# Optimization experiments

Measured on AMD Instinct MI355X. Metric: run time of the kernel, lower is better.

The kernel has to match this reference:

```python
import jax, jax.numpy as jnp
import numpy as np

D_MODEL = 1024
N_HEAD = 16
D_K = D_MODEL // N_HEAD
D_FF = 2048
N_EXPERTS = 8
TOP_K = 2
B = 4
S = 1024
LN_EPS = 1e-5


def _layer_norm(x, g, b):
    mu = jnp.mean(x, axis=-1, keepdims=True)
    var = jnp.mean(jnp.square(x - mu), axis=-1, keepdims=True)
    return (x - mu) * jax.lax.rsqrt(var + LN_EPS) * g + b


def setup_inputs() -> dict:
    key = jax.random.key(0)
    ks = jax.random.split(key, 16)
    std = 0.02
    inp = {
        "x": jax.random.normal(ks[0], (B, S, D_MODEL), dtype=jnp.float32),
        "mask": jnp.ones((B, S, S), dtype=jnp.int32),
        "ln1_g": jnp.ones((D_MODEL,), jnp.float32),
        "ln1_b": jnp.zeros((D_MODEL,), jnp.float32),
        "wq": jax.random.normal(ks[1], (D_MODEL, D_MODEL), jnp.float32) * std,
        "wk": jax.random.normal(ks[2], (D_MODEL, D_MODEL), jnp.float32) * std,
        "wv": jax.random.normal(ks[3], (D_MODEL, D_MODEL), jnp.float32) * std,
        "wo": jax.random.normal(ks[4], (D_MODEL, D_MODEL), jnp.float32) * std,
        "wqd": jax.random.normal(ks[5], (D_MODEL, D_MODEL), jnp.float32) * std,
        "wkd": jax.random.normal(ks[6], (D_MODEL, D_MODEL), jnp.float32) * std,
        "wvd": jax.random.normal(ks[7], (D_MODEL, D_MODEL), jnp.float32) * std,
        "wod": jax.random.normal(ks[8], (D_MODEL, D_MODEL), jnp.float32) * std,
        "w_gate": jax.random.normal(ks[9], (D_MODEL, 2), jnp.float32) * std,
        "ln2_g": jnp.ones((D_MODEL,), jnp.float32),
        "ln2_b": jnp.zeros((D_MODEL,), jnp.float32),
        "w_router": jax.random.normal(ks[10], (D_MODEL, N_EXPERTS), jnp.float32) * std,
        "e_w1": jax.random.normal(ks[11], (N_EXPERTS, D_MODEL, D_FF), jnp.float32) * std,
        "e_w2": jax.random.normal(ks[12], (N_EXPERTS, D_FF, D_MODEL), jnp.float32) * std,
    }
    return inp


def _attention(x, mask, wq, wk, wv, wo, wqd, wkd, wvd, wod, w_gate):
    b, s, d = x.shape

    def split_heads(t):  # [b,s,d] -> [b,h,s,dk]
        return t.reshape(b, s, N_HEAD, D_K).transpose(0, 2, 1, 3)

    def merge_heads(t):  # [b,h,s,dk] -> [b,s,d]
        return t.transpose(0, 2, 1, 3).reshape(b, s, d)

    # dense attention branch
    q = split_heads(x @ wq)
    k = split_heads(x @ wk)
    v = split_heads(x @ wv)
    scores = jnp.einsum("bhqd,bhkd->bhqk", q, k) / jnp.sqrt(jnp.float32(D_K))
    scores = jnp.where(mask[:, None, :, :] == 0, jnp.float32(-1e9), scores)
    probs = jax.nn.softmax(scores, axis=-1)
    dense = merge_heads(jnp.einsum("bhqk,bhkd->bhqd", probs, v)) @ wo

    # linear delta attention branch (O(n))
    qd = split_heads(x @ wqd)
    kd = split_heads(x @ wkd)
    vd = split_heads(x @ wvd)
    q_lin = jax.nn.relu(qd)
    k_lin = jax.nn.relu(kd)
    # NOTE: original uses the *non-relu* k for the context matrix
    context = jnp.einsum("bhsd,bhse->bhde", kd, vd)  # [b,h,dk,dk]
    out = jnp.einsum("bhsd,bhde->bhse", q_lin, context)
    z = jnp.sum(q_lin * jnp.sum(k_lin, axis=-2, keepdims=True), axis=-1, keepdims=True) + 1e-6
    delta = merge_heads(out / z) @ wod

    gate = jax.nn.softmax(x @ w_gate, axis=-1)  # [b,s,2]
    return gate[..., 0:1] * dense + gate[..., 1:2] * delta


def _moe(x, w_router, e_w1, e_w2):
    b, s, d = x.shape
    xt = x.reshape(b * s, d)  # tokens
    logits = xt @ w_router  # [N, E]
    topk_logits, topk_idx = jax.lax.top_k(logits, TOP_K)
    topk_w = jax.nn.softmax(topk_logits, axis=-1)  # [N, K]
    # dense combine weights [N, E] (equivalent to masked gather/scatter-add)
    n = xt.shape[0]
    comb = jnp.zeros((n, N_EXPERTS), xt.dtype).at[jnp.arange(n)[:, None], topk_idx].add(topk_w)
    # all tokens through all experts (jit-friendly dense dispatch)
    h = jax.nn.gelu(jnp.einsum("nd,edf->enf", xt, e_w1), approximate=False)
    y = jnp.einsum("enf,efd->end", h, e_w2)
    out = jnp.einsum("end,ne->nd", y, comb)
    return out.reshape(b, s, d)


def reference(x, mask, ln1_g, ln1_b, wq, wk, wv, wo, wqd, wkd, wvd, wod, w_gate,
              ln2_g, ln2_b, w_router, e_w1, e_w2):
    x = x + _attention(_layer_norm(x, ln1_g, ln1_b), mask,
                       wq, wk, wv, wo, wqd, wkd, wvd, wod, w_gate)
    x = x + _moe(_layer_norm(x, ln2_g, ln2_b), w_router, e_w1, e_w2)
    return x
```

## Files before the change

kernel.cpp:

```cpp
#include <hip/hip_runtime.h>
#include <stdint.h>


typedef __attribute__((ext_vector_type(8))) short short8;
typedef __attribute__((ext_vector_type(4))) float floatx4;

#define DMODEL 1024
#define SEQ    1024
#define NHEAD  16
#define DK     64
#define DFF    2048
#define NEXP   8
#define MAXTILE 144

__device__ __forceinline__ float bf2f(unsigned short h){
  union{unsigned u;float f;}v; v.u=((unsigned)h)<<16; return v.f;
}
__device__ __forceinline__ unsigned short f2bf(float f){
  union{float f;unsigned u;}v; v.f=f;
  unsigned r=(v.u + 0x7FFFu + ((v.u>>16)&1u))>>16; return (unsigned short)r;
}
__device__ __forceinline__ void splitbf(float v, unsigned short& hi, unsigned short& lo){
  hi = f2bf(v); lo = f2bf(v - bf2f(hi));
}

__device__ __forceinline__ void glds16(const unsigned short* g, unsigned short* l){
  __builtin_amdgcn_global_load_lds(
      (const __attribute__((address_space(1))) void*)g,
      (__attribute__((address_space(3))) void*)l, 16, 0, 0);
}

__device__ __forceinline__ float block_sum(float v, float* red){
  for(int off=32;off;off>>=1) v += __shfl_down(v,off,64);
  int w = threadIdx.x>>6;
  __syncthreads();
  if((threadIdx.x&63)==0) red[w]=v;
  __syncthreads();
  return red[0]+red[1]+red[2]+red[3];
}

__global__ __launch_bounds__(256) void k_maskpack(
    const int* __restrict__ mask, unsigned long long* __restrict__ mp){
  int gw = blockIdx.x*4 + (threadIdx.x>>6);
  int lane = threadIdx.x&63;
  unsigned long long bm = __ballot(mask[(long)gw*64 + lane] != 0);
  if(lane==0) mp[gw]=bm;
}

__global__ __launch_bounds__(256) void k_transpose_f2(
    const float* __restrict__ src, unsigned short* __restrict__ dh,
    unsigned short* __restrict__ dl, long srs, long drs, long sbs, long dbs){
  __shared__ float t[32][33];
  src += (long)blockIdx.z*sbs; dh += (long)blockIdx.z*dbs; dl += (long)blockIdx.z*dbs;
  int c0 = blockIdx.x*32, r0 = blockIdx.y*32;
  int tx = threadIdx.x & 31, ty = threadIdx.x >> 5;
  for(int i=0;i<32;i+=8)
    t[ty+i][tx] = src[(long)(r0+ty+i)*srs + (c0+tx)];
  __syncthreads();
  for(int i=0;i<32;i+=8){
    unsigned short hi,lo; splitbf(t[tx][ty+i],hi,lo);
    long idx = (long)(c0+ty+i)*drs + (r0+tx);
    dh[idx]=hi; dl[idx]=lo;
  }
}

__global__ __launch_bounds__(256) void k_transpose_f(
    const float* __restrict__ src, unsigned short* __restrict__ dst,
    long srs, long drs, long sbs, long dbs){
  __shared__ float t[32][33];
  src += (long)blockIdx.z*sbs; dst += (long)blockIdx.z*dbs;
  int c0 = blockIdx.x*32, r0 = blockIdx.y*32;
  int tx = threadIdx.x & 31, ty = threadIdx.x >> 5;
  for(int i=0;i<32;i+=8)
    t[ty+i][tx] = src[(long)(r0+ty+i)*srs + (c0+tx)];
  __syncthreads();
  for(int i=0;i<32;i+=8)
    dst[(long)(c0+ty+i)*drs + (r0+tx)] = f2bf(t[tx][ty+i]);
}

__global__ __launch_bounds__(256) void k_vt(
    const unsigned short* __restrict__ qh, const unsigned short* __restrict__ ql,
    unsigned short* __restrict__ vth, unsigned short* __restrict__ vtl){
  __shared__ unsigned short th[32][33], tl[32][33];
  int z = blockIdx.z, b = z>>4, h = z&15;
  int s0 = blockIdx.x*32, d0 = blockIdx.y*32;
  int tx = threadIdx.x & 31, ty = threadIdx.x >> 5;
  for(int i=0;i<32;i+=8){
    long src = (long)(b*SEQ + s0+ty+i)*6144 + 2048 + h*DK + d0+tx;
    th[ty+i][tx] = qh[src]; tl[ty+i][tx] = ql[src];
  }
  __syncthreads();
  for(int i=0;i<32;i+=8){
    long dst = ((long)z*DK + d0+ty+i)*SEQ + s0+tx;
    vth[dst] = th[tx][ty+i]; vtl[dst] = tl[tx][ty+i];
  }
}

__global__ __launch_bounds__(256) void k_ln1(
    const float* __restrict__ x, const float* __restrict__ g,
    const float* __restrict__ b, unsigned short* __restrict__ oh,
    unsigned short* __restrict__ ol){
  __shared__ float red[4];
  int t = blockIdx.x, tid = threadIdx.x;
  long base = (long)t*DMODEL + tid*4;
  floatx4 xv = *(const floatx4*)(x + base);
  float v[4] = {xv[0], xv[1], xv[2], xv[3]};
  float s = block_sum(v[0]+v[1]+v[2]+v[3], red);
  float mu = s * (1.f/DMODEL);
  float q=0.f;
  for(int i=0;i<4;i++){ float d=v[i]-mu; q+=d*d; }
  q = block_sum(q, red);
  float inv = rsqrtf(q*(1.f/DMODEL) + 1e-5f);
  for(int i=0;i<4;i++){
    int d = tid*4+i;
    unsigned short hi,lo; splitbf((v[i]-mu)*inv*g[d] + b[d], hi, lo);
    oh[base+i]=hi; ol[base+i]=lo;
  }
}

template<int SPLIT>
__global__ __launch_bounds__(256) void k_gemm128_ss(
    const unsigned short* __restrict__ Ah, const unsigned short* __restrict__ Al,
    const unsigned short* __restrict__ Bh, const unsigned short* __restrict__ Bl,
    unsigned short* __restrict__ Ch, unsigned short* __restrict__ Cl,
    float* __restrict__ Cf, int K, int lda, int ldb, int ldc, int gridN){
  __shared__ unsigned short Ash[128*32], Asl[128*32];
  __shared__ unsigned short Bsh[128*32], Bsl[128*32];
  int nwg = gridDim.x, bid = blockIdx.x;
  int swz = (bid & 7)*(nwg >> 3) + (bid >> 3);
  int bx = swz % gridN, by = swz / gridN;
  int m0 = by*128, n0 = bx*128;
  int tid = threadIdx.x, w = tid>>6, lane = tid&63;
  int qm = lane&15, quad = lane>>4;
  int wr = w>>1, wc = w&1;
  int srow = (w<<4) + (lane>>2);
  int schunk = (lane&3)*8;
  int sdst = srow*32 + schunk;
  const unsigned short* pA0h = Ah + (long)(m0+srow   )*lda + schunk;
  const unsigned short* pA1h = Ah + (long)(m0+srow+64)*lda + schunk;
  const unsigned short* pA0l = Al + (long)(m0+srow   )*lda + schunk;
  const unsigned short* pA1l = Al + (long)(m0+srow+64)*lda + schunk;
  const unsigned short* pB0h = Bh + (long)(n0+srow   )*ldb + schunk;
  const unsigned short* pB1h = Bh + (long)(n0+srow+64)*ldb + schunk;
  const unsigned short* pB0l = Bl + (long)(n0+srow   )*ldb + schunk;
  const unsigned short* pB1l = Bl + (long)(n0+srow+64)*ldb + schunk;

  floatx4 acc[4][4];
  #pragma unroll
  for(int m=0;m<4;m++)
    #pragma unroll
    for(int n=0;n<4;n++) acc[m][n] = (floatx4){0.f,0.f,0.f,0.f};

  for(int k0=0;k0<K;k0+=32){
    __syncthreads();
    glds16(pA0h+k0, Ash+sdst); glds16(pA1h+k0, Ash+sdst+2048);
    glds16(pA0l+k0, Asl+sdst); glds16(pA1l+k0, Asl+sdst+2048);
    glds16(pB0h+k0, Bsh+sdst); glds16(pB1h+k0, Bsh+sdst+2048);
    glds16(pB0l+k0, Bsl+sdst); glds16(pB1l+k0, Bsl+sdst+2048);
    __syncthreads();
    short8 ah[4], al[4], bh[4], bl[4];
    #pragma unroll
    for(int m=0;m<4;m++){
      int ar = (wr*64 + m*16 + qm)*32 + quad*8;
      ah[m] = *(const short8*)(Ash+ar);
      al[m] = *(const short8*)(Asl+ar);
    }
    #pragma unroll
    for(int n=0;n<4;n++){
      int br = (wc*64 + n*16 + qm)*32 + quad*8;
      bh[n] = *(const short8*)(Bsh+br);
      bl[n] = *(const short8*)(Bsl+br);
    }
    #pragma unroll
    for(int m=0;m<4;m++)
      #pragma unroll
      for(int n=0;n<4;n++){
        acc[m][n] = __builtin_amdgcn_mfma_f32_16x16x32_bf16(ah[m],bh[n],acc[m][n],0,0,0);
        acc[m][n] = __builtin_amdgcn_mfma_f32_16x16x32_bf16(ah[m],bl[n],acc[m][n],0,0,0);
        acc[m][n] = __builtin_amdgcn_mfma_f32_16x16x32_bf16(al[m],bh[n],acc[m][n],0,0,0);
      }
  }
  #pragma unroll
  for(int m=0;m<4;m++){
    int row = m0 + wr*64 + m*16 + quad*4;
    #pragma unroll
    for(int r=0;r<4;r++){
      long rb = (long)(row+r)*ldc + n0 + wc*64;
      #pragma unroll
      for(int n=0;n<4;n++){
        float v = acc[m][n][r];
        if(SPLIT){
          unsigned short hi,lo; splitbf(v,hi,lo);
          Ch[rb+n*16+qm]=hi; Cl[rb+n*16+qm]=lo;
        }else{
          Cf[rb+n*16+qm]=v;
        }
      }
    }
  }
}

__global__ __launch_bounds__(256) void k_gate(
    const unsigned short* __restrict__ hh, const unsigned short* __restrict__ hl,
    const float* __restrict__ wg, float* __restrict__ gates){
  int token = blockIdx.x*4 + (threadIdx.x>>6);
  int lane = threadIdx.x&63;
  long hb = (long)token*DMODEL + lane*16;
  const float* w = wg + lane*16*2;
  float s0=0.f, s1=0.f;
  for(int i=0;i<16;i++){
    float hv = bf2f(hh[hb+i]) + bf2f(hl[hb+i]);
    s0 += hv*w[2*i]; s1 += hv*w[2*i+1];
  }
  for(int off=32;off;off>>=1){ s0+=__shfl_down(s0,off,64); s1+=__shfl_down(s1,off,64); }
  if(lane==0){
    float m=fmaxf(s0,s1), e0=__expf(s0-m), e1=__expf(s1-m), inv=1.f/(e0+e1);
    gates[token*2]=e0*inv; gates[token*2+1]=e1*inv;
  }
}

__global__ __launch_bounds__(256) void k_attn_flash3(
    const unsigned short* __restrict__ qh, const unsigned short* __restrict__ qlp,
    const unsigned short* __restrict__ vth, const unsigned short* __restrict__ vtl,
    const unsigned long long* __restrict__ mp, unsigned short* __restrict__ dmh,
    unsigned short* __restrict__ dml){
  __shared__ unsigned short Ksh[64*64], Ksl[64*64];
  __shared__ unsigned short Vsh[64*64], Vsl[64*64];
  __shared__ unsigned short PWh[4*16*64], PWl[4*16*64];
  int bh = blockIdx.y, b = bh>>4, h = bh&15;
  int tid = threadIdx.x, w = tid>>6, lane = tid&63;
  int qm = lane&15, quad = (lane>>4)&3;
  int q0 = blockIdx.x*64 + w*16;
  long qrow = (long)(b*SEQ+q0+qm)*6144 + h*DK;
  short8 a_qh0 = *(const short8*)(qh +qrow+quad*8);
  short8 a_qh1 = *(const short8*)(qh +qrow+32+quad*8);
  short8 a_ql0 = *(const short8*)(qlp+qrow+quad*8);
  short8 a_ql1 = *(const short8*)(qlp+qrow+32+quad*8);
  float m[4], l[4];
  floatx4 o0={0,0,0,0}, o1={0,0,0,0}, o2={0,0,0,0}, o3={0,0,0,0};
  #pragma unroll
  for(int r=0;r<4;r++){ m[r]=-3.0e38f; l[r]=0.f; }
  const unsigned long long* mrow = mp + ((long)b*SEQ + q0 + quad*4)*16;

  int r8 = lane>>3;
  int c8 = (lane&7) ^ r8;
  int d0 = w*512 + lane*8;
  const unsigned short* pKh0 = qh  + (long)(b*SEQ + w*8 + r8)*6144 + 1024 + h*DK + c8*8;
  const unsigned short* pKl0 = qlp + (long)(b*SEQ + w*8 + r8)*6144 + 1024 + h*DK + c8*8;
  const unsigned short* pKh1 = pKh0 + 32L*6144;
  const unsigned short* pKl1 = pKl0 + 32L*6144;
  const unsigned short* pVh0 = vth + ((long)bh*DK + w*8 + r8)*SEQ + c8*8;
  const unsigned short* pVl0 = vtl + ((long)bh*DK + w*8 + r8)*SEQ + c8*8;
  const unsigned short* pVh1 = pVh0 + 32L*SEQ;
  const unsigned short* pVl1 = pVl0 + 32L*SEQ;
  int q7 = qm&7;

  for(int kt=0; kt<SEQ; kt+=64){
    __syncthreads();
    long ko = (long)kt*6144;
    glds16(pKh0+ko, Ksh+d0); glds16(pKh1+ko, Ksh+d0+2048);
    glds16(pKl0+ko, Ksl+d0); glds16(pKl1+ko, Ksl+d0+2048);
    glds16(pVh0+kt, Vsh+d0); glds16(pVh1+kt, Vsh+d0+2048);
    glds16(pVl0+kt, Vsl+d0); glds16(pVl1+kt, Vsl+d0+2048);
    __syncthreads();

    int wd = kt>>6;
    unsigned long long mws[4] = {mrow[wd], mrow[16+wd], mrow[32+wd], mrow[48+wd]};
    floatx4 s[4];
    #pragma unroll
    for(int st=0;st<4;st++){
      int krow = (st*16+qm)*64;
      short8 kh0 = *(const short8*)(Ksh + krow + ((quad    ^q7)<<3));
      short8 kh1 = *(const short8*)(Ksh + krow + (((4|quad)^q7)<<3));
      short8 kl0 = *(const short8*)(Ksl + krow + ((quad    ^q7)<<3));
      short8 kl1 = *(const short8*)(Ksl + krow + (((4|quad)^q7)<<3));
      floatx4 acc = {0,0,0,0};
      acc = __builtin_amdgcn_mfma_f32_16x16x32_bf16(a_qh0,kh0,acc,0,0,0);
      acc = __builtin_amdgcn_mfma_f32_16x16x32_bf16(a_qh1,kh1,acc,0,0,0);
      acc = __builtin_amdgcn_mfma_f32_16x16x32_bf16(a_qh0,kl0,acc,0,0,0);
      acc = __builtin_amdgcn_mfma_f32_16x16x32_bf16(a_qh1,kl1,acc,0,0,0);
      acc = __builtin_amdgcn_mfma_f32_16x16x32_bf16(a_ql0,kh0,acc,0,0,0);
      acc = __builtin_amdgcn_mfma_f32_16x16x32_bf16(a_ql1,kh1,acc,0,0,0);
      s[st] = acc;
    }
    #pragma unroll
    for(int r=0;r<4;r++){
      float v0 = ((mws[r]>>(   qm))&1) ? s[0][r]*0.125f : -1e9f;
      float v1 = ((mws[r]>>(16+qm))&1) ? s[1][r]*0.125f : -1e9f;
      float v2 = ((mws[r]>>(32+qm))&1) ? s[2][r]*0.125f : -1e9f;
      float v3 = ((mws[r]>>(48+qm))&1) ? s[3][r]*0.125f : -1e9f;
      float tm = fmaxf(fmaxf(v0,v1), fmaxf(v2,v3));
      tm = fmaxf(tm, __shfl_xor(tm,1,16));
      tm = fmaxf(tm, __shfl_xor(tm,2,16));
      tm = fmaxf(tm, __shfl_xor(tm,4,16));
      tm = fmaxf(tm, __shfl_xor(tm,8,16));
      float nm = fmaxf(m[r], tm);
      float al = __expf(m[r]-nm);
      m[r] = nm;
      float p0=__expf(v0-nm), p1=__expf(v1-nm), p2=__expf(v2-nm), p3=__expf(v3-nm);
      float rs = p0+p1+p2+p3;
      rs += __shfl_xor(rs,1,16); rs += __shfl_xor(rs,2,16);
      rs += __shfl_xor(rs,4,16); rs += __shfl_xor(rs,8,16);
      l[r] = l[r]*al + rs;
      o0[r]*=al; o1[r]*=al; o2[r]*=al; o3[r]*=al;
      int row = quad*4+r, rsw = row&7;
      int pb = w*1024 + row*64 + (qm&7);
      unsigned short hi,lo;
      splitbf(p0,hi,lo); PWh[pb + ((( (qm>>3))^rsw)<<3)]=hi; PWl[pb + ((( (qm>>3))^rsw)<<3)]=lo;
      splitbf(p1,hi,lo); PWh[pb + (((2|(qm>>3))^rsw)<<3)]=hi; PWl[pb + (((2|(qm>>3))^rsw)<<3)]=lo;
      splitbf(p2,hi,lo); PWh[pb + (((4|(qm>>3))^rsw)<<3)]=hi; PWl[pb + (((4|(qm>>3))^rsw)<<3)]=lo;
      splitbf(p3,hi,lo); PWh[pb + (((6|(qm>>3))^rsw)<<3)]=hi; PWl[pb + (((6|(qm>>3))^rsw)<<3)]=lo;
    }
    __builtin_amdgcn_wave_barrier();
    int prb = w*1024 + qm*64;
    short8 ph0 = *(const short8*)(PWh + prb + ((quad    ^q7)<<3));
    short8 ph1 = *(const short8*)(PWh + prb + (((4|quad)^q7)<<3));
    short8 pl0 = *(const short8*)(PWl + prb + ((quad    ^q7)<<3));
    short8 pl1 = *(const short8*)(PWl + prb + (((4|quad)^q7)<<3));
    __builtin_amdgcn_wave_barrier();
    {
      int c0 = (quad    ^q7)<<3;
      int c1 = ((4|quad)^q7)<<3;
      int vr0 = (0*16+qm)*64, vr1 = (1*16+qm)*64, vr2 = (2*16+qm)*64, vr3 = (3*16+qm)*64;
      short8 v0h0=*(const short8*)(Vsh+vr0+c0), v0h1=*(const short8*)(Vsh+vr0+c1);
      short8 v1h0=*(const short8*)(Vsh+vr1+c0), v1h1=*(const short8*)(Vsh+vr1+c1);
      short8 v2h0=*(const short8*)(Vsh+vr2+c0), v2h1=*(const short8*)(Vsh+vr2+c1);
      short8 v3h0=*(const short8*)(Vsh+vr3+c0), v3h1=*(const short8*)(Vsh+vr3+c1);
      short8 v0l0=*(const short8*)(Vsl+vr0+c0), v0l1=*(const short8*)(Vsl+vr0+c1);
      short8 v1l0=*(const short8*)(Vsl+vr1+c0), v1l1=*(const short8*)(Vsl+vr1+c1);
      short8 v2l0=*(const short8*)(Vsl+vr2+c0), v2l1=*(const short8*)(Vsl+vr2+c1);
      short8 v3l0=*(const short8*)(Vsl+vr3+c0), v3l1=*(const short8*)(Vsl+vr3+c1);
      o0 = __builtin_amdgcn_mfma_f32_16x16x32_bf16(ph0,v0h0,o0,0,0,0);
      o0 = __builtin_amdgcn_mfma_f32_16x16x32_bf16(ph1,v0h1,o0,0,0,0);
      o0 = __builtin_amdgcn_mfma_f32_16x16x32_bf16(ph0,v0l0,o0,0,0,0);
      o0 = __builtin_amdgcn_mfma_f32_16x16x32_bf16(ph1,v0l1,o0,0,0,0);
      o0 = __builtin_amdgcn_mfma_f32_16x16x32_bf16(pl0,v0h0,o0,0,0,0);
      o0 = __builtin_amdgcn_mfma_f32_16x16x32_bf16(pl1,v0h1,o0,0,0,0);
      o1 = __builtin_amdgcn_mfma_f32_16x16x32_bf16(ph0,v1h0,o1,0,0,0);
      o1 = __builtin_amdgcn_mfma_f32_16x16x32_bf16(ph1,v1h1,o1,0,0,0);
      o1 = __builtin_amdgcn_mfma_f32_16x16x32_bf16(ph0,v1l0,o1,0,0,0);
      o1 = __builtin_amdgcn_mfma_f32_16x16x32_bf16(ph1,v1l1,o1,0,0,0);
      o1 = __builtin_amdgcn_mfma_f32_16x16x32_bf16(pl0,v1h0,o1,0,0,0);
      o1 = __builtin_amdgcn_mfma_f32_16x16x32_bf16(pl1,v1h1,o1,0,0,0);
      o2 = __builtin_amdgcn_mfma_f32_16x16x32_bf16(ph0,v2h0,o2,0,0,0);
      o2 = __builtin_amdgcn_mfma_f32_16x16x32_bf16(ph1,v2h1,o2,0,0,0);
      o2 = __builtin_amdgcn_mfma_f32_16x16x32_bf16(ph0,v2l0,o2,0,0,0);
      o2 = __builtin_amdgcn_mfma_f32_16x16x32_bf16(ph1,v2l1,o2,0,0,0);
      o2 = __builtin_amdgcn_mfma_f32_16x16x32_bf16(pl0,v2h0,o2,0,0,0);
      o2 = __builtin_amdgcn_mfma_f32_16x16x32_bf16(pl1,v2h1,o2,0,0,0);
      o3 = __builtin_amdgcn_mfma_f32_16x16x32_bf16(ph0,v3h0,o3,0,0,0);
      o3 = __builtin_amdgcn_mfma_f32_16x16x32_bf16(ph1,v3h1,o3,0,0,0);
      o3 = __builtin_amdgcn_mfma_f32_16x16x32_bf16(ph0,v3l0,o3,0,0,0);
      o3 = __builtin_amdgcn_mfma_f32_16x16x32_bf16(ph1,v3l1,o3,0,0,0);
      o3 = __builtin_amdgcn_mfma_f32_16x16x32_bf16(pl0,v3h0,o3,0,0,0);
      o3 = __builtin_amdgcn_mfma_f32_16x16x32_bf16(pl1,v3h1,o3,0,0,0);
    }
  }
  #pragma unroll
  for(int r=0;r<4;r++){
    float inv = 1.f/l[r];
    long rb = ((long)(b*SEQ + q0 + quad*4 + r))*DMODEL + h*DK;
    unsigned short hi,lo;
    splitbf(o0[r]*inv,hi,lo); dmh[rb+   qm]=hi; dml[rb+   qm]=lo;
    splitbf(o1[r]*inv,hi,lo); dmh[rb+16+qm]=hi; dml[rb+16+qm]=lo;
    splitbf(o2[r]*inv,hi,lo); dmh[rb+32+qm]=hi; dml[rb+32+qm]=lo;
    splitbf(o3[r]*inv,hi,lo); dmh[rb+48+qm]=hi; dml[rb+48+qm]=lo;
  }
}

__global__ __launch_bounds__(256) void k_delta_ctx(
    const unsigned short* __restrict__ qh, const unsigned short* __restrict__ qlp,
    float* __restrict__ ctx, float* __restrict__ ksum){
  int bh = blockIdx.x, b=bh>>4, h=bh&15;
  __shared__ unsigned short kdh[64][64], kdl[64][64], vdh[64][64], vdl[64][64];
  int tid = threadIdx.x;
  int i = tid>>2, jg = (tid&3)*16;
  float acc[16]; for(int k=0;k<16;k++) acc[k]=0.f;
  float ks = 0.f;
  int rr = tid>>2, cg = (tid&3)*16;
  for(int s0=0;s0<SEQ;s0+=64){
    __syncthreads();
    long base = (long)(b*SEQ + s0 + rr)*6144 + h*DK;
    *(short8*)(&kdh[rr][cg])   = *(const short8*)(qh  + base + 4096 + cg);
    *(short8*)(&kdh[rr][cg+8]) = *(const short8*)(qh  + base + 4096 + cg + 8);
    *(short8*)(&kdl[rr][cg])   = *(const short8*)(qlp + base + 4096 + cg);
    *(short8*)(&kdl[rr][cg+8]) = *(const short8*)(qlp + base + 4096 + cg + 8);
    *(short8*)(&vdh[rr][cg])   = *(const short8*)(qh  + base + 5120 + cg);
    *(short8*)(&vdh[rr][cg+8]) = *(const short8*)(qh  + base + 5120 + cg + 8);
    *(short8*)(&vdl[rr][cg])   = *(const short8*)(qlp + base + 5120 + cg);
    *(short8*)(&vdl[rr][cg+8]) = *(const short8*)(qlp + base + 5120 + cg + 8);
    __syncthreads();
    for(int s=0;s<64;s++){
      float kv = bf2f(kdh[s][i]) + bf2f(kdl[s][i]);
      if((tid&3)==0) ks += fmaxf(kv,0.f);
      for(int j=0;j<16;j++)
        acc[j] += kv * (bf2f(vdh[s][jg+j]) + bf2f(vdl[s][jg+j]));
    }
  }
  long cb = (long)bh*DK*DK;
  for(int j=0;j<16;j++) ctx[cb + (long)i*DK + jg + j] = acc[j];
  if((tid&3)==0) ksum[bh*DK + i] = ks;
}

__global__ __launch_bounds__(256) void k_delta_out(
    const unsigned short* __restrict__ qh, const unsigned short* __restrict__ qlp,
    const float* __restrict__ ctx, const float* __restrict__ ksum,
    unsigned short* __restrict__ dlh, unsigned short* __restrict__ dll){
  int tok = blockIdx.x, b = tok>>10;
  int tid = threadIdx.x;
  __shared__ float ql[DMODEL];
  long sb = (long)tok*6144 + 3072;
  for(int c=tid;c<DMODEL;c+=256)
    ql[c] = fmaxf(bf2f(qh[sb+c]) + bf2f(qlp[sb+c]), 0.f);
  __syncthreads();
  int h = tid>>4, dg = (tid&15)*4;
  int bh = b*NHEAD + h;
  const float* C = ctx + (long)bh*DK*DK;
  const float* KS = ksum + bh*DK;
  float a0=0,a1=0,a2=0,a3=0,z=0;
  for(int d=0;d<DK;d++){
    float q = ql[h*DK + d];
    z += q * KS[d];
    const float* cr = C + d*DK + dg;
    a0 += q*cr[0]; a1 += q*cr[1]; a2 += q*cr[2]; a3 += q*cr[3];
  }
  float inv = 1.f/(z + 1e-6f);
  long db = (long)tok*DMODEL + h*DK + dg;
  unsigned short hi,lo;
  splitbf(a0*inv,hi,lo); dlh[db  ]=hi; dll[db  ]=lo;
  splitbf(a1*inv,hi,lo); dlh[db+1]=hi; dll[db+1]=lo;
  splitbf(a2*inv,hi,lo); dlh[db+2]=hi; dll[db+2]=lo;
  splitbf(a3*inv,hi,lo); dlh[db+3]=hi; dll[db+3]=lo;
}

__global__ __launch_bounds__(256) void k_comb_router(
    const float* __restrict__ x, const float* __restrict__ dp,
    const float* __restrict__ dlp, const float* __restrict__ gates,
    const float* __restrict__ g, const float* __restrict__ bb,
    const float* __restrict__ wr, unsigned short* __restrict__ h2b,
    float* __restrict__ topw, int* __restrict__ topi, int* __restrict__ counts){
  __shared__ float red[4];
  __shared__ float ered[4][8];
  int t = blockIdx.x, tid = threadIdx.x;
  float g0 = gates[t*2], g1 = gates[t*2+1];
  long base = (long)t*DMODEL + tid*4;
  floatx4 xv = *(const floatx4*)(x + base);
  float v[4];
  for(int i=0;i<4;i++) v[i] = xv[i] + g0*dp[base+i] + g1*dlp[base+i];
  float s = block_sum(v[0]+v[1]+v[2]+v[3], red);
  float mu = s*(1.f/DMODEL);
  float q=0.f; for(int i=0;i<4;i++){ float d=v[i]-mu; q+=d*d; }
  q = block_sum(q, red);
  float inv = rsqrtf(q*(1.f/DMODEL)+1e-5f);
  float a[8]; for(int e=0;e<8;e++) a[e]=0.f;
  for(int i=0;i<4;i++){
    int d = tid*4+i;
    float hv = (v[i]-mu)*inv*g[d] + bb[d];
    h2b[base+i] = f2bf(hv);
    const float* wrow = wr + (long)d*NEXP;
    for(int e=0;e<8;e++) a[e] += hv*wrow[e];
  }
  for(int off=32;off;off>>=1)
    for(int e=0;e<8;e++) a[e] += __shfl_down(a[e],off,64);
  int w = tid>>6;
  if((tid&63)==0) for(int e=0;e<8;e++) ered[w][e]=a[e];
  __syncthreads();
  if(tid==0){
    float lg[8];
    for(int e=0;e<8;e++) lg[e]=ered[0][e]+ered[1][e]+ered[2][e]+ered[3][e];
    int i0=0; for(int e=1;e<8;e++) if(lg[e]>lg[i0]) i0=e;
    int i1=-1; for(int e=0;e<8;e++){ if(e==i0) continue; if(i1<0||lg[e]>lg[i1]) i1=e; }
    float mm=fmaxf(lg[i0],lg[i1]), e0=__expf(lg[i0]-mm), e1=__expf(lg[i1]-mm), s2=1.f/(e0+e1);
    topw[t*2]=e0*s2; topw[t*2+1]=e1*s2;
    topi[t*2]=i0; topi[t*2+1]=i1;
    atomicAdd(&counts[i0],1); atomicAdd(&counts[i1],1);
  }
}

__global__ void k_meta(const int* __restrict__ counts, int* offs, int* tE,
                       int* tR0, int* tR1, int* ntp, int* cursor){
  if(threadIdx.x==0){
    int o=0, nt=0;
    for(int e=0;e<NEXP;e++){
      offs[e]=o; cursor[e]=0;
      int n=counts[e];
      for(int t=0;t<(n+127)/128;t++){ tE[nt]=e; tR0[nt]=o+t*128; tR1[nt]=o+n; nt++; }
      o+=n;
    }
    offs[NEXP]=o; ntp[0]=nt;
  }
}

__global__ __launch_bounds__(256) void k_scatter(
    const int* __restrict__ topi, const int* __restrict__ offs,
    int* cursor, int* perm, int* slotof){
  int token = blockIdx.x*256 + threadIdx.x;
  for(int k=0;k<2;k++){
    int e = topi[token*2+k];
    int pos = atomicAdd(&cursor[e],1);
    int slot = offs[e]+pos;
    perm[slot]=token; slotof[token*2+k]=slot;
  }
}

template<int GELU, int GATHER>
__global__ __launch_bounds__(256) void k_moe128(
    const unsigned short* __restrict__ A, const unsigned short* __restrict__ BtA,
    unsigned short* __restrict__ C, const int* __restrict__ perm,
    const int* __restrict__ ntp, const int* __restrict__ tE,
    const int* __restrict__ tR0, const int* __restrict__ tR1,
    int K, int N){
  int bz = blockIdx.y;
  if(bz >= ntp[0]) return;
  int e = tE[bz], r0t = tR0[bz], r1t = tR1[bz];
  __shared__ unsigned short As[128*32], Bs[128*32];
  int tid = threadIdx.x, w = tid>>6, lane = tid&63;
  int qm = lane&15, quad = lane>>4;
  int wr = w>>1, wc = w&1;
  int n0 = blockIdx.x*128;
  int srow = (w<<4) + (lane>>2);
  int schunk = (lane&3)*8;
  int sdst = srow*32 + schunk;
  int gr0 = r0t + srow, gr1 = gr0 + 64;
  int gc0 = gr0 < 8191 ? gr0 : 8191;
  int gc1 = gr1 < 8191 ? gr1 : 8191;
  const unsigned short* pA0;
  const unsigned short* pA1;
  if(GATHER){
    pA0 = A + (long)perm[gc0]*K + schunk;
    pA1 = A + (long)perm[gc1]*K + schunk;
  }else{
    pA0 = A + (long)gc0*K + schunk;
    pA1 = A + (long)gc1*K + schunk;
  }
  const unsigned short* Bt = BtA + (long)e*N*K;
  const unsigned short* pB0 = Bt + (long)(n0+srow   )*K + schunk;
  const unsigned short* pB1 = Bt + (long)(n0+srow+64)*K + schunk;

  floatx4 acc[4][4];
  #pragma unroll
  for(int m=0;m<4;m++)
    #pragma unroll
    for(int n=0;n<4;n++) acc[m][n] = (floatx4){0.f,0.f,0.f,0.f};

  for(int k0=0;k0<K;k0+=32){
    __syncthreads();
    glds16(pA0+k0, As+sdst); glds16(pA1+k0, As+sdst+2048);
    glds16(pB0+k0, Bs+sdst); glds16(pB1+k0, Bs+sdst+2048);
    __syncthreads();
    short8 af[4], bf[4];
    #pragma unroll
    for(int m=0;m<4;m++)
      af[m] = *(const short8*)(As + (wr*64 + m*16 + qm)*32 + quad*8);
    #pragma unroll
    for(int n=0;n<4;n++)
      bf[n] = *(const short8*)(Bs + (wc*64 + n*16 + qm)*32 + quad*8);
    #pragma unroll
    for(int m=0;m<4;m++)
      #pragma unroll
      for(int n=0;n<4;n++)
        acc[m][n] = __builtin_amdgcn_mfma_f32_16x16x32_bf16(af[m],bf[n],acc[m][n],0,0,0);
  }
  #pragma unroll
  for(int m=0;m<4;m++){
    int row = r0t + wr*64 + m*16 + quad*4;
    #pragma unroll
    for(int r=0;r<4;r++){
      if(row+r < r1t){
        long rb = (long)(row+r)*N + n0 + wc*64;
        #pragma unroll
        for(int n=0;n<4;n++){
          float xx = acc[m][n][r];
          if(GELU) xx = 0.5f*xx*(1.f+erff(xx*0.70710678f));
          C[rb+n*16+qm] = f2bf(xx);
        }
      }
    }
  }
}

__global__ __launch_bounds__(256) void k_final(
    const float* __restrict__ x, const float* __restrict__ dp,
    const float* __restrict__ dlp, const float* __restrict__ gates,
    const unsigned short* __restrict__ Y, const int* __restrict__ slotof,
    const float* __restrict__ topw, float* __restrict__ out){
  int t = blockIdx.x, tid = threadIdx.x;
  int s0 = slotof[t*2], s1 = slotof[t*2+1];
  float w0 = topw[t*2], w1 = topw[t*2+1];
  float g0 = gates[t*2], g1 = gates[t*2+1];
  long base = (long)t*DMODEL + tid*4;
  const unsigned short* y0 = Y + (long)s0*DMODEL + tid*4;
  const unsigned short* y1 = Y + (long)s1*DMODEL + tid*4;
  floatx4 xv = *(const floatx4*)(x + base);
  for(int i=0;i<4;i++)
    out[base+i] = xv[i] + g0*dp[base+i] + g1*dlp[base+i]
                        + w0*bf2f(y0[i]) + w1*bf2f(y1[i]);
}

extern "C" void kernel_launch(void* const* d_in, const int* in_sizes, int n_in,
                              void* d_out, int out_size, void* d_ws, size_t ws_size,
                              hipStream_t stream){
  const float* x    = (const float*)d_in[0];
  const int*   mask = (const int*)d_in[1];
  const float* ln1g = (const float*)d_in[2];
  const float* ln1b = (const float*)d_in[3];
  const float* wq   = (const float*)d_in[4];
  const float* wk   = (const float*)d_in[5];
  const float* wv   = (const float*)d_in[6];
  const float* wo   = (const float*)d_in[7];
  const float* wqd  = (const float*)d_in[8];
  const float* wkd  = (const float*)d_in[9];
  const float* wvd  = (const float*)d_in[10];
  const float* wod  = (const float*)d_in[11];
  const float* wg   = (const float*)d_in[12];
  const float* ln2g = (const float*)d_in[13];
  const float* ln2b = (const float*)d_in[14];
  const float* wr   = (const float*)d_in[15];
  const float* ew1  = (const float*)d_in[16];
  const float* ew2  = (const float*)d_in[17];
  float* out = (float*)d_out;

  char* p = (char*)d_ws;
  auto alloc = [&](size_t b)->char*{ char* r=p; p += (b + 255) & ~(size_t)255; return r; };
  unsigned short* WtAllh = (unsigned short*)alloc(6144L*1024*2);
  unsigned short* WtAlll = (unsigned short*)alloc(6144L*1024*2);
  unsigned short* WoTh   = (unsigned short*)alloc(1024L*1024*2);
  unsigned short* WoTl   = (unsigned short*)alloc(1024L*1024*2);
  unsigned short* WodTh  = (unsigned short*)alloc(1024L*1024*2);
  unsigned short* WodTl  = (unsigned short*)alloc(1024L*1024*2);
  unsigned short* eW1T   = (unsigned short*)alloc(8L*2048*1024*2);
  unsigned short* eW2T   = (unsigned short*)alloc(8L*1024*2048*2);
  unsigned short* h1h    = (unsigned short*)alloc(4096L*1024*2);
  unsigned short* h1l    = (unsigned short*)alloc(4096L*1024*2);
  unsigned short* qkvh   = (unsigned short*)alloc(4096L*6144*2);
  unsigned short* qkvl   = (unsigned short*)alloc(4096L*6144*2);
  unsigned short* dmh    = (unsigned short*)alloc(4096L*1024*2);
  unsigned short* dml    = (unsigned short*)alloc(4096L*1024*2);
  unsigned short* dlh    = (unsigned short*)alloc(4096L*1024*2);
  unsigned short* dll    = (unsigned short*)alloc(4096L*1024*2);
  float* ctx   = (float*)alloc(64L*64*64*4);
  float* ksum  = (float*)alloc(64L*64*4);
  float* gates = (float*)alloc(4096L*2*4);
  unsigned short* h2b = (unsigned short*)alloc(4096L*1024*2);
  float* topw = (float*)alloc(4096L*2*4);
  int* topi   = (int*)alloc(4096L*2*4);
  int* slotof = (int*)alloc(4096L*2*4);
  int* perm   = (int*)alloc(8192L*4);
  int* counts = (int*)alloc(64*4);
  int* cursor = (int*)alloc(64*4);
  int* offs   = (int*)alloc(64*4);
  int* ntp    = (int*)alloc(64*4);
  int* tE     = (int*)alloc(MAXTILE*4);
  int* tR0    = (int*)alloc(MAXTILE*4);
  int* tR1    = (int*)alloc(MAXTILE*4);
  unsigned long long* mpack = (unsigned long long*)alloc(4L*1024*16*8);
  if ((size_t)(p - (char*)d_ws) > ws_size) return;

  unsigned short* vTh = h1h;
  unsigned short* vTl = h1l;
  float* dproj  = (float*)qkvh;
  float* dlproj = (float*)(qkvh + 8388608);
  unsigned short* H = qkvl;
  unsigned short* Y = dmh;

  dim3 tb(256);
  k_maskpack<<<16384,tb,0,stream>>>(mask, mpack);
  k_transpose_f2<<<dim3(32,32,1),tb,0,stream>>>(wq,  WtAllh+0L*1048576, WtAlll+0L*1048576, 1024,1024, 0,0);
  k_transpose_f2<<<dim3(32,32,1),tb,0,stream>>>(wk,  WtAllh+1L*1048576, WtAlll+1L*1048576, 1024,1024, 0,0);
  k_transpose_f2<<<dim3(32,32,1),tb,0,stream>>>(wv,  WtAllh+2L*1048576, WtAlll+2L*1048576, 1024,1024, 0,0);
  k_transpose_f2<<<dim3(32,32,1),tb,0,stream>>>(wqd, WtAllh+3L*1048576, WtAlll+3L*1048576, 1024,1024, 0,0);
  k_transpose_f2<<<dim3(32,32,1),tb,0,stream>>>(wkd, WtAllh+4L*1048576, WtAlll+4L*1048576, 1024,1024, 0,0);
  k_transpose_f2<<<dim3(32,32,1),tb,0,stream>>>(wvd, WtAllh+5L*1048576, WtAlll+5L*1048576, 1024,1024, 0,0);
  k_transpose_f2<<<dim3(32,32,1),tb,0,stream>>>(wo,  WoTh,  WoTl,  1024,1024, 0,0);
  k_transpose_f2<<<dim3(32,32,1),tb,0,stream>>>(wod, WodTh, WodTl, 1024,1024, 0,0);
  k_transpose_f<<<dim3(64,32,8),tb,0,stream>>>(ew1, eW1T, 2048,1024, 1024L*2048, 2048L*1024);
  k_transpose_f<<<dim3(32,64,8),tb,0,stream>>>(ew2, eW2T, 1024,2048, 2048L*1024, 1024L*2048);
  k_ln1<<<4096,tb,0,stream>>>(x, ln1g, ln1b, h1h, h1l);
  k_gemm128_ss<1><<<dim3(1536),tb,0,stream>>>(h1h,h1l, WtAllh,WtAlll, qkvh,qkvl,nullptr,
                                              1024, 1024, 1024, 6144, 48);
  k_gate<<<1024,tb,0,stream>>>(h1h, h1l, wg, gates);
  k_vt<<<dim3(32,2,64),tb,0,stream>>>(qkvh, qkvl, vTh, vTl);
  k_attn_flash3<<<dim3(16,64),tb,0,stream>>>(qkvh, qkvl, vTh, vTl, mpack, dmh, dml);
  k_delta_ctx<<<64,tb,0,stream>>>(qkvh, qkvl, ctx, ksum);
  k_delta_out<<<4096,tb,0,stream>>>(qkvh, qkvl, ctx, ksum, dlh, dll);
  k_gemm128_ss<0><<<dim3(256),tb,0,stream>>>(dmh,dml, WoTh,WoTl,  nullptr,nullptr,dproj,
                                             1024, 1024, 1024, 1024, 8);
  k_gemm128_ss<0><<<dim3(256),tb,0,stream>>>(dlh,dll, WodTh,WodTl, nullptr,nullptr,dlproj,
                                             1024, 1024, 1024, 1024, 8);
  hipMemsetAsync(counts, 0, NEXP*sizeof(int), stream);
  k_comb_router<<<4096,tb,0,stream>>>(x, dproj, dlproj, gates, ln2g, ln2b, wr,
                                      h2b, topw, topi, counts);
  k_meta<<<1,64,0,stream>>>(counts, offs, tE, tR0, tR1, ntp, cursor);
  k_scatter<<<16,tb,0,stream>>>(topi, offs, cursor, perm, slotof);
  k_moe128<1,1><<<dim3(16,72),tb,0,stream>>>(h2b, eW1T, H, perm, ntp, tE, tR0, tR1,
                                             1024, 2048);
  k_moe128<0,0><<<dim3(8,72),tb,0,stream>>>(H, eW2T, Y, perm, ntp, tE, tR0, tR1,
                                            2048, 1024);
  k_final<<<4096,tb,0,stream>>>(x, dproj, dlproj, gates, Y, slotof, topw, out);
}
```

Measured before the change: 1.171 ms.

## Move delta context to MFMA with transposed K/V and swizzle GEMM LDS layout

Result: faster. 1.060 ms (-9.4%).

```diff
diff --git a/kernel.cpp b/kernel.cpp
--- a/kernel.cpp
+++ b/kernel.cpp
@@ -80,13 +80,13 @@
 
 __global__ __launch_bounds__(256) void k_vt(
     const unsigned short* __restrict__ qh, const unsigned short* __restrict__ ql,
-    unsigned short* __restrict__ vth, unsigned short* __restrict__ vtl){
+    unsigned short* __restrict__ vth, unsigned short* __restrict__ vtl, long coff){
   __shared__ unsigned short th[32][33], tl[32][33];
   int z = blockIdx.z, b = z>>4, h = z&15;
   int s0 = blockIdx.x*32, d0 = blockIdx.y*32;
   int tx = threadIdx.x & 31, ty = threadIdx.x >> 5;
   for(int i=0;i<32;i+=8){
-    long src = (long)(b*SEQ + s0+ty+i)*6144 + 2048 + h*DK + d0+tx;
+    long src = (long)(b*SEQ + s0+ty+i)*6144 + coff + h*DK + d0+tx;
     th[ty+i][tx] = qh[src]; tl[ty+i][tx] = ql[src];
   }
   __syncthreads();
@@ -133,17 +133,19 @@
   int tid = threadIdx.x, w = tid>>6, lane = tid&63;
   int qm = lane&15, quad = lane>>4;
   int wr = w>>1, wc = w&1;
-  int srow = (w<<4) + (lane>>2);
-  int schunk = (lane&3)*8;
-  int sdst = srow*32 + schunk;
-  const unsigned short* pA0h = Ah + (long)(m0+srow   )*lda + schunk;
-  const unsigned short* pA1h = Ah + (long)(m0+srow+64)*lda + schunk;
-  const unsigned short* pA0l = Al + (long)(m0+srow   )*lda + schunk;
-  const unsigned short* pA1l = Al + (long)(m0+srow+64)*lda + schunk;
-  const unsigned short* pB0h = Bh + (long)(n0+srow   )*ldb + schunk;
-  const unsigned short* pB1h = Bh + (long)(n0+srow+64)*ldb + schunk;
-  const unsigned short* pB0l = Bl + (long)(n0+srow   )*ldb + schunk;
-  const unsigned short* pB1l = Bl + (long)(n0+srow+64)*ldb + schunk;
+  int lg = lane>>3, pp = lane&7, px = pp ^ lg;
+  int rowl = (w<<4) + (lg<<1) + (px>>2);
+  int c4s = (px&3)*8;
+  int sdst = w*512 + lane*8;
+  const unsigned short* pA0h = Ah + (long)(m0+rowl   )*lda + c4s;
+  const unsigned short* pA1h = Ah + (long)(m0+rowl+64)*lda + c4s;
+  const unsigned short* pA0l = Al + (long)(m0+rowl   )*lda + c4s;
+  const unsigned short* pA1l = Al + (long)(m0+rowl+64)*lda + c4s;
+  const unsigned short* pB0h = Bh + (long)(n0+rowl   )*ldb + c4s;
+  const unsigned short* pB1h = Bh + (long)(n0+rowl+64)*ldb + c4s;
+  const unsigned short* pB0l = Bl + (long)(n0+rowl   )*ldb + c4s;
+  const unsigned short* pB1l = Bl + (long)(n0+rowl+64)*ldb + c4s;
+  int fc = (((((qm&1)<<2)|quad) ^ (qm>>1))<<3);
 
   floatx4 acc[4][4];
   #pragma unroll
@@ -161,13 +163,13 @@
     short8 ah[4], al[4], bh[4], bl[4];
     #pragma unroll
     for(int m=0;m<4;m++){
-      int ar = (wr*64 + m*16 + qm)*32 + quad*8;
+      int ar = (wr*32 + m*8 + (qm>>1))*64 + fc;
       ah[m] = *(const short8*)(Ash+ar);
       al[m] = *(const short8*)(Asl+ar);
     }
     #pragma unroll
     for(int n=0;n<4;n++){
-      int br = (wc*64 + n*16 + qm)*32 + quad*8;
+      int br = (wc*32 + n*8 + (qm>>1))*64 + fc;
       bh[n] = *(const short8*)(Bsh+br);
       bl[n] = *(const short8*)(Bsl+br);
     }
@@ -368,38 +370,55 @@
   }
 }
 
-__global__ __launch_bounds__(256) void k_delta_ctx(
-    const unsigned short* __restrict__ qh, const unsigned short* __restrict__ qlp,
-    float* __restrict__ ctx, float* __restrict__ ksum){
-  int bh = blockIdx.x, b=bh>>4, h=bh&15;
-  __shared__ unsigned short kdh[64][64], kdl[64][64], vdh[64][64], vdl[64][64];
-  int tid = threadIdx.x;
-  int i = tid>>2, jg = (tid&3)*16;
-  float acc[16]; for(int k=0;k<16;k++) acc[k]=0.f;
-  float ks = 0.f;
-  int rr = tid>>2, cg = (tid&3)*16;
-  for(int s0=0;s0<SEQ;s0+=64){
-    __syncthreads();
-    long base = (long)(b*SEQ + s0 + rr)*6144 + h*DK;
-    *(short8*)(&kdh[rr][cg])   = *(const short8*)(qh  + base + 4096 + cg);
-    *(short8*)(&kdh[rr][cg+8]) = *(const short8*)(qh  + base + 4096 + cg + 8);
-    *(short8*)(&kdl[rr][cg])   = *(const short8*)(qlp + base + 4096 + cg);
-    *(short8*)(&kdl[rr][cg+8]) = *(const short8*)(qlp + base + 4096 + cg + 8);
-    *(short8*)(&vdh[rr][cg])   = *(const short8*)(qh  + base + 5120 + cg);
-    *(short8*)(&vdh[rr][cg+8]) = *(const short8*)(qh  + base + 5120 + cg + 8);
-    *(short8*)(&vdl[rr][cg])   = *(const short8*)(qlp + base + 5120 + cg);
-    *(short8*)(&vdl[rr][cg+8]) = *(const short8*)(qlp + base + 5120 + cg + 8);
-    __syncthreads();
-    for(int s=0;s<64;s++){
-      float kv = bf2f(kdh[s][i]) + bf2f(kdl[s][i]);
-      if((tid&3)==0) ks += fmaxf(kv,0.f);
-      for(int j=0;j<16;j++)
-        acc[j] += kv * (bf2f(vdh[s][jg+j]) + bf2f(vdl[s][jg+j]));
+__global__ __launch_bounds__(256) void k_delta_ctx2(
+    const unsigned short* __restrict__ kdTh, const unsigned short* __restrict__ kdTl,
+    const unsigned short* __restrict__ vdTh, const unsigned short* __restrict__ vdTl,
+    float* __restrict__ ctx){
+  int bh = blockIdx.x;
+  int tid = threadIdx.x, w = tid>>6, lane = tid&63;
+  int qm = lane&15, quad = lane>>4;
+  long abase = ((long)bh*DK + w*16 + qm)*SEQ + quad*8;
+  long bbase = ((long)bh*DK + qm)*SEQ + quad*8;
+  floatx4 acc[4];
+  #pragma unroll
+  for(int n=0;n<4;n++) acc[n] = (floatx4){0.f,0.f,0.f,0.f};
+  #pragma unroll 2
+  for(int s0=0;s0<SEQ;s0+=32){
+    short8 ah = *(const short8*)(kdTh + abase + s0);
+    short8 al = *(const short8*)(kdTl + abase + s0);
+    #pragma unroll
+    for(int n=0;n<4;n++){
+      short8 bh8 = *(const short8*)(vdTh + bbase + (long)n*16*SEQ + s0);
+      short8 bl8 = *(const short8*)(vdTl + bbase + (long)n*16*SEQ + s0);
+      acc[n] = __builtin_amdgcn_mfma_f32_16x16x32_bf16(ah,bh8,acc[n],0,0,0);
+      acc[n] = __builtin_amdgcn_mfma_f32_16x16x32_bf16(ah,bl8,acc[n],0,0,0);
+      acc[n] = __builtin_amdgcn_mfma_f32_16x16x32_bf16(al,bh8,acc[n],0,0,0);
     }
   }
   long cb = (long)bh*DK*DK;
-  for(int j=0;j<16;j++) ctx[cb + (long)i*DK + jg + j] = acc[j];
-  if((tid&3)==0) ksum[bh*DK + i] = ks;
+  #pragma unroll
+  for(int n=0;n<4;n++)
+    #pragma unroll
+    for(int r=0;r<4;r++)
+      ctx[cb + (long)(w*16 + quad*4 + r)*DK + n*16 + qm] = acc[n][r];
+}
+
+__global__ __launch_bounds__(256) void k_ksum(
+    const unsigned short* __restrict__ kdTh, const unsigned short* __restrict__ kdTl,
+    float* __restrict__ ksum){
+  int bh = blockIdx.x, tid = threadIdx.x;
+  int d = tid>>2, part = tid&3;
+  long base = ((long)bh*DK + d)*SEQ + part*256;
+  float s = 0.f;
+  for(int i=0;i<256;i+=8){
+    short8 hq = *(const short8*)(kdTh+base+i);
+    short8 lq = *(const short8*)(kdTl+base+i);
+    #pragma unroll
+    for(int j=0;j<8;j++)
+      s += fmaxf(bf2f((unsigned short)hq[j]) + bf2f((unsigned short)lq[j]), 0.f);
+  }
+  s += __shfl_xor(s,1,64); s += __shfl_xor(s,2,64);
+  if(part==0) ksum[bh*DK + d] = s;
 }
 
 __global__ __launch_bounds__(256) void k_delta_out(
@@ -518,24 +537,26 @@
   int qm = lane&15, quad = lane>>4;
   int wr = w>>1, wc = w&1;
   int n0 = blockIdx.x*128;
-  int srow = (w<<4) + (lane>>2);
-  int schunk = (lane&3)*8;
-  int sdst = srow*32 + schunk;
-  int gr0 = r0t + srow, gr1 = gr0 + 64;
+  int lg = lane>>3, pp = lane&7, px = pp ^ lg;
+  int rowl = (w<<4) + (lg<<1) + (px>>2);
+  int c4s = (px&3)*8;
+  int sdst = w*512 + lane*8;
+  int fc = (((((qm&1)<<2)|quad) ^ (qm>>1))<<3);
+  int gr0 = r0t + rowl, gr1 = gr0 + 64;
   int gc0 = gr0 < 8191 ? gr0 : 8191;
   int gc1 = gr1 < 8191 ? gr1 : 8191;
   const unsigned short* pA0;
   const unsigned short* pA1;
   if(GATHER){
-    pA0 = A + (long)perm[gc0]*K + schunk;
-    pA1 = A + (long)perm[gc1]*K + schunk;
+    pA0 = A + (long)perm[gc0]*K + c4s;
+    pA1 = A + (long)perm[gc1]*K + c4s;
   }else{
-    pA0 = A + (long)gc0*K + schunk;
-    pA1 = A + (long)gc1*K + schunk;
+    pA0 = A + (long)gc0*K + c4s;
+    pA1 = A + (long)gc1*K + c4s;
   }
   const unsigned short* Bt = BtA + (long)e*N*K;
-  const unsigned short* pB0 = Bt + (long)(n0+srow   )*K + schunk;
-  const unsigned short* pB1 = Bt + (long)(n0+srow+64)*K + schunk;
+  const unsigned short* pB0 = Bt + (long)(n0+rowl   )*K + c4s;
+  const unsigned short* pB1 = Bt + (long)(n0+rowl+64)*K + c4s;
 
   floatx4 acc[4][4];
   #pragma unroll
@@ -551,10 +572,10 @@
     short8 af[4], bf[4];
     #pragma unroll
     for(int m=0;m<4;m++)
-      af[m] = *(const short8*)(As + (wr*64 + m*16 + qm)*32 + quad*8);
+      af[m] = *(const short8*)(As + (wr*32 + m*8 + (qm>>1))*64 + fc);
     #pragma unroll
     for(int n=0;n<4;n++)
-      bf[n] = *(const short8*)(Bs + (wc*64 + n*16 + qm)*32 + quad*8);
+      bf[n] = *(const short8*)(Bs + (wc*32 + n*8 + (qm>>1))*64 + fc);
     #pragma unroll
     for(int m=0;m<4;m++)
       #pragma unroll
@@ -658,6 +679,10 @@
 
   unsigned short* vTh = h1h;
   unsigned short* vTl = h1l;
+  unsigned short* kdTh = dlh;
+  unsigned short* kdTl = dll;
+  unsigned short* vdTh = dmh;
+  unsigned short* vdTl = dml;
   float* dproj  = (float*)qkvh;
   float* dlproj = (float*)(qkvh + 8388608);
   unsigned short* H = qkvl;
@@ -679,9 +704,12 @@
   k_gemm128_ss<1><<<dim3(1536),tb,0,stream>>>(h1h,h1l, WtAllh,WtAlll, qkvh,qkvl,nullptr,
                                               1024, 1024, 1024, 6144, 48);
   k_gate<<<1024,tb,0,stream>>>(h1h, h1l, wg, gates);
-  k_vt<<<dim3(32,2,64),tb,0,stream>>>(qkvh, qkvl, vTh, vTl);
+  k_vt<<<dim3(32,2,64),tb,0,stream>>>(qkvh, qkvl, vTh, vTl, 2048);
+  k_vt<<<dim3(32,2,64),tb,0,stream>>>(qkvh, qkvl, kdTh, kdTl, 4096);
+  k_vt<<<dim3(32,2,64),tb,0,stream>>>(qkvh, qkvl, vdTh, vdTl, 5120);
+  k_delta_ctx2<<<64,tb,0,stream>>>(kdTh, kdTl, vdTh, vdTl, ctx);
+  k_ksum<<<64,tb,0,stream>>>(kdTh, kdTl, ksum);
   k_attn_flash3<<<dim3(16,64),tb,0,stream>>>(qkvh, qkvl, vTh, vTl, mpack, dmh, dml);
-  k_delta_ctx<<<64,tb,0,stream>>>(qkvh, qkvl, ctx, ksum);
   k_delta_out<<<4096,tb,0,stream>>>(qkvh, qkvl, ctx, ksum, dlh, dll);
   k_gemm128_ss<0><<<dim3(256),tb,0,stream>>>(dmh,dml, WoTh,WoTl,  nullptr,nullptr,dproj,
                                              1024, 1024, 1024, 1024, 8);
```
